# Performance work log

Hardware: AMD Instinct MI355X
Metric: run time of the kernel (lower is better)

Reference implementation:

```python
import jax, jax.numpy as jnp
import numpy as np

BOX = 100.0      # points live in [0, BOX)^3
STRIDE = 128     # > BOX/voxel_size, used for linearizing 3D voxel coords


def setup_inputs() -> dict:
    key = jax.random.key(0)
    k1, k2 = jax.random.split(key)
    N, C = 2_000_000, 32
    positions = jax.random.uniform(k1, (N, 3), dtype=jnp.float32) * BOX
    features = jax.random.normal(k2, (N, C), dtype=jnp.float32)
    voxel_size = jnp.ones((), dtype=jnp.float32)
    return {"positions": positions, "features": features, "voxel_size": voxel_size}


def reference(positions, features, voxel_size):
    """VoxelPooling(position_fn='center', feature_fn='max').

    Output is padded to N rows (M <= N real voxels); `valid` marks real voxels.
    Voxel grid is aligned to the origin; pooled position is the voxel center.
    """
    N = positions.shape[0]
    # integer voxel coordinates (positions are non-negative here)
    coords = jnp.floor(positions / voxel_size).astype(jnp.int32)           # [N,3]
    lin = coords[:, 0] + STRIDE * coords[:, 1] + STRIDE * STRIDE * coords[:, 2]  # [N]
    # compact unique voxels; jit-compatible with fixed size=N, pad with -1
    uniq, inv = jnp.unique(lin, size=N, fill_value=-1, return_inverse=True)
    # per-voxel max over features (empty segments get dtype-min, masked below)
    pooled_features = jax.ops.segment_max(features, inv, num_segments=N)   # [N,C]
    # decode voxel coords from linear key -> voxel centers
    cz = uniq // (STRIDE * STRIDE)
    rem = uniq % (STRIDE * STRIDE)
    cy = rem // STRIDE
    cx = rem % STRIDE
    centers = (jnp.stack([cx, cy, cz], axis=-1).astype(positions.dtype) + 0.5) * voxel_size
    valid = uniq >= 0                                                      # [N]
    pooled_positions = jnp.where(valid[:, None], centers, 0.0)
    pooled_features = jnp.where(valid[:, None], pooled_features, 0.0)
    return pooled_positions, pooled_features, valid
```

## Files before the change

kernel.cpp:

```cpp
#include <hip/hip_runtime.h>
#include <stdint.h>

#define STRIDE 128
#define NVOX (STRIDE * STRIDE * STRIDE)
#define BINVOX 512
#define NBIN (NVOX / BINVOX)
#define HB 256
#define HT 1024

typedef unsigned long long u64;

__device__ __forceinline__ uint32_t enc_f32(float f) {
  uint32_t u = __float_as_uint(f);
  return (u & 0x80000000u) ? ~u : (u | 0x80000000u);
}
__device__ __forceinline__ float dec_f32(uint32_t e) {
  uint32_t u = (e & 0x80000000u) ? (e & 0x7fffffffu) : ~e;
  return __uint_as_float(u);
}

__global__ __launch_bounds__(HT) void k_hist(const float* __restrict__ pos,
                                             const float* __restrict__ vs_p,
                                             int* __restrict__ lin_arr,
                                             uint32_t* __restrict__ hist, int n) {
  __shared__ uint32_t h[NBIN];
  int b = blockIdx.x, t = threadIdx.x;
  #pragma unroll
  for (int k = t; k < NBIN; k += HT) h[k] = 0u;
  __syncthreads();
  int chunk = (n + HB - 1) / HB;
  int i0 = b * chunk, i1 = min(n, i0 + chunk);
  float vs = vs_p[0];
  for (int i = i0 + t; i < i1; i += HT) {
    float x = pos[3 * (size_t)i + 0];
    float y = pos[3 * (size_t)i + 1];
    float z = pos[3 * (size_t)i + 2];
    int lin = (int)floorf(x / vs) + STRIDE * (int)floorf(y / vs) +
              STRIDE * STRIDE * (int)floorf(z / vs);
    lin_arr[i] = lin;
    atomicAdd(&h[lin >> 9], 1u);
  }
  __syncthreads();
  #pragma unroll
  for (int k = t; k < NBIN; k += HT) hist[(size_t)b * NBIN + k] = h[k];
}

__global__ void k_scanA(const uint32_t* __restrict__ hist, uint32_t* __restrict__ base2,
                        uint32_t* __restrict__ bin_tot) {
  int bin = blockIdx.x * blockDim.x + threadIdx.x;
  uint32_t run = 0;
  #pragma unroll 8
  for (int b = 0; b < HB; ++b) {
    uint32_t v = hist[(size_t)b * NBIN + bin];
    base2[(size_t)b * NBIN + bin] = run;
    run += v;
  }
  bin_tot[bin] = run;
}

__global__ __launch_bounds__(1024) void k_scan4k(const uint32_t* __restrict__ in,
                                                 uint32_t* __restrict__ out,
                                                 uint32_t* __restrict__ Mp) {
  __shared__ uint32_t s[1024];
  int t = threadIdx.x;
  uint32_t v[4], sum = 0;
  #pragma unroll
  for (int j = 0; j < 4; ++j) { v[j] = in[t * 4 + j]; sum += v[j]; }
  s[t] = sum;
  __syncthreads();
  for (int off = 1; off < 1024; off <<= 1) {
    uint32_t a = (t >= off) ? s[t - off] : 0u;
    __syncthreads();
    s[t] += a;
    __syncthreads();
  }
  uint32_t run = s[t] - sum;
  #pragma unroll
  for (int j = 0; j < 4; ++j) { out[t * 4 + j] = run; run += v[j]; }
  if (Mp != nullptr && t == 1023) Mp[0] = s[1023];
}

__global__ __launch_bounds__(HT) void k_part(const int* __restrict__ lin_arr,
                                             const uint32_t* __restrict__ bin_base,
                                             const uint32_t* __restrict__ base2,
                                             uint32_t* __restrict__ pairs, int n) {
  __shared__ uint32_t cur[NBIN];
  int b = blockIdx.x, t = threadIdx.x;
  #pragma unroll
  for (int k = t; k < NBIN; k += HT)
    cur[k] = bin_base[k] + base2[(size_t)b * NBIN + k];
  __syncthreads();
  int chunk = (n + HB - 1) / HB;
  int i0 = b * chunk, i1 = min(n, i0 + chunk);
  for (int i = i0 + t; i < i1; i += HT) {
    int lin = lin_arr[i];
    uint32_t slot = atomicAdd(&cur[lin >> 9], 1u);
    pairs[slot] = ((uint32_t)(lin & (BINVOX - 1)) << 21) | (uint32_t)i;
  }
}

__global__ void k_occ(const uint32_t* __restrict__ pairs,
                      const uint32_t* __restrict__ bin_base,
                      const uint32_t* __restrict__ bin_tot,
                      uint32_t* __restrict__ bins_bw, uint32_t* __restrict__ occ_cnt) {
  __shared__ uint32_t bw[16];
  int bin = blockIdx.x, t = threadIdx.x;
  if (t < 16) bw[t] = 0u;
  __syncthreads();
  uint32_t cnt = bin_tot[bin], start = bin_base[bin];
  for (uint32_t u = (uint32_t)t; u < cnt; u += blockDim.x) {
    uint32_t vb = pairs[start + u] >> 21;
    atomicOr(&bw[vb >> 5], 1u << (vb & 31));
  }
  __syncthreads();
  if (t < 16) bins_bw[(size_t)bin * 16 + t] = bw[t];
  if (t == 0) {
    uint32_t o = 0;
    #pragma unroll
    for (int w = 0; w < 16; ++w) o += __popc(bw[w]);
    occ_cnt[bin] = o;
  }
}

__global__ __launch_bounds__(1024) void k_pool(
    const float* __restrict__ feat, const float* __restrict__ vs_p,
    const uint32_t* __restrict__ pairs, const uint32_t* __restrict__ bin_base,
    const uint32_t* __restrict__ bin_tot, const uint32_t* __restrict__ occ_base,
    const uint32_t* __restrict__ bins_bw,
    float* __restrict__ out_pos, float* __restrict__ out_feat,
    float* __restrict__ out_valid) {
  __shared__ uint32_t smax[BINVOX * 32];
  __shared__ uint32_t sbw[16];
  int bin = blockIdx.x;
  int t = threadIdx.x;
  uint32_t cnt = bin_tot[bin];
  if (cnt == 0) return;
  uint32_t start = bin_base[bin];

  #pragma unroll
  for (int k = 0; k < 16; ++k) smax[t + k * 1024] = 0u;
  if (t < 16) sbw[t] = bins_bw[(size_t)bin * 16 + t];
  __syncthreads();

  int g = t >> 5;
  int ch = t & 31;
  uint32_t last = cnt - 1;
  for (uint32_t u = (uint32_t)g; u < cnt; u += 128) {
    uint32_t u1 = min(u + 32u, last), u2 = min(u + 64u, last), u3 = min(u + 96u, last);
    uint32_t p0 = pairs[start + u],  p1 = pairs[start + u1];
    uint32_t p2 = pairs[start + u2], p3 = pairs[start + u3];
    float v0 = feat[(size_t)(p0 & 0x1FFFFFu) * 32 + ch];
    float v1 = feat[(size_t)(p1 & 0x1FFFFFu) * 32 + ch];
    float v2 = feat[(size_t)(p2 & 0x1FFFFFu) * 32 + ch];
    float v3 = feat[(size_t)(p3 & 0x1FFFFFu) * 32 + ch];
    atomicMax(&smax[(p0 >> 21) * 32 + ch], enc_f32(v0));
    atomicMax(&smax[(p1 >> 21) * 32 + ch], enc_f32(v1));
    atomicMax(&smax[(p2 >> 21) * 32 + ch], enc_f32(v2));
    atomicMax(&smax[(p3 >> 21) * 32 + ch], enc_f32(v3));
  }
  __syncthreads();

  int vb = t >> 1, half = t & 1;
  uint32_t w = sbw[vb >> 5];
  uint32_t bit = (uint32_t)vb & 31u;
  if ((w >> bit) & 1u) {
    uint32_t lr = __popc(w & ((1u << bit) - 1u));
    for (int ww = 0; ww < (vb >> 5); ++ww) lr += __popc(sbw[ww]);
    uint32_t rank = occ_base[bin] + lr;
    float4* orow = (float4*)(out_feat + (size_t)rank * 32 + half * 16);
    #pragma unroll
    for (int j = 0; j < 4; ++j) {
      const uint32_t* sp = &smax[vb * 32 + half * 16 + j * 4];
      float4 o;
      o.x = dec_f32(sp[0]); o.y = dec_f32(sp[1]);
      o.z = dec_f32(sp[2]); o.w = dec_f32(sp[3]);
      orow[j] = o;
    }
    if (half == 0) {
      float vs = vs_p[0];
      int lin = bin * BINVOX + vb;
      int cx = lin & 127, cy = (lin >> 7) & 127, cz = lin >> 14;
      out_pos[(size_t)rank * 3 + 0] = ((float)cx + 0.5f) * vs;
      out_pos[(size_t)rank * 3 + 1] = ((float)cy + 0.5f) * vs;
      out_pos[(size_t)rank * 3 + 2] = ((float)cz + 0.5f) * vs;
      out_valid[rank] = 1.0f;
    }
  }
}

__global__ void k_tail(const uint32_t* __restrict__ Mp, float* __restrict__ out_pos,
                       float* __restrict__ out_feat, float* __restrict__ out_valid, int n) {
  size_t gid = (size_t)blockIdx.x * blockDim.x + threadIdx.x;
  int row = (int)(gid >> 3);
  int q = (int)(gid & 7);
  if (row >= n) return;
  uint32_t M = Mp[0];
  if ((uint32_t)row < M) return;
  ((float4*)out_feat)[(size_t)row * 8 + q] = make_float4(0.f, 0.f, 0.f, 0.f);
  if (q == 0) {
    out_pos[(size_t)row * 3 + 0] = 0.f;
    out_pos[(size_t)row * 3 + 1] = 0.f;
    out_pos[(size_t)row * 3 + 2] = 0.f;
    out_valid[row] = 0.f;
  }
}

extern "C" void kernel_launch(void* const* d_in, const int* in_sizes, int n_in,
                              void* d_out, int out_size, void* d_ws, size_t ws_size,
                              hipStream_t stream) {
  const float* pos  = (const float*)d_in[0];
  const float* feat = (const float*)d_in[1];
  const float* vs   = (const float*)d_in[2];
  int n = in_sizes[0] / 3;

  float*    out_pos   = (float*)d_out;
  uint32_t* out_feat  = (uint32_t*)(out_pos + (size_t)n * 3);
  float*    out_valid = (float*)((float*)out_feat + (size_t)n * 32);

  size_t scratch_u32 = 2 * (size_t)n + 2 * (size_t)HB * NBIN + 4 * (size_t)NBIN +
                       16 * (size_t)NBIN;
  uint32_t* scratch  = out_feat + (size_t)n * 32 - scratch_u32;
  int*      lin      = (int*)scratch;
  uint32_t* pairs    = scratch + n;
  uint32_t* hist     = pairs + n;
  uint32_t* base2    = hist + (size_t)HB * NBIN;
  uint32_t* bin_tot  = base2 + (size_t)HB * NBIN;
  uint32_t* bin_base = bin_tot + NBIN;
  uint32_t* occ_cnt  = bin_base + NBIN;
  uint32_t* occ_base = occ_cnt + NBIN;
  uint32_t* bins_bw  = occ_base + NBIN;

  uint32_t* Mp = (uint32_t*)d_ws;

  k_hist<<<HB, HT, 0, stream>>>(pos, vs, lin, hist, n);
  k_scanA<<<NBIN / 256, 256, 0, stream>>>(hist, base2, bin_tot);
  k_scan4k<<<1, 1024, 0, stream>>>(bin_tot, bin_base, nullptr);
  k_part<<<HB, HT, 0, stream>>>(lin, bin_base, base2, pairs, n);
  k_occ<<<NBIN, 256, 0, stream>>>(pairs, bin_base, bin_tot, bins_bw, occ_cnt);
  k_scan4k<<<1, 1024, 0, stream>>>(occ_cnt, occ_base, Mp);
  k_pool<<<NBIN, 1024, 0, stream>>>(feat, vs, pairs, bin_base, bin_tot, occ_base,
                                    bins_bw, out_pos, (float*)out_feat, out_valid);
  k_tail<<<(int)(((size_t)n * 8 + 255) / 256), 256, 0, stream>>>(
      Mp, out_pos, (float*)out_feat, out_valid, n);
}
```

Before: 230.7 us.

## Track voxel occupancy with a byte map and fuse both scans into one

Occupancy is now recorded in a per-voxel byte map written during the histogram pass. It is counted by popcount in the per-bin scan and rebuilt as 64-bit ballot masks in the pool kernel. This removes the separate k_occ pass over the pairs array and the second single-block scan, because bin counts and occupancy counts are packed into one 64-bit value and scanned together. The pool loop also unrolls to eight gathers per iteration for more memory-level parallelism. In exchange it adds a 2 MB memset and scattered byte writes in k_hist, plus higher register pressure in k_pool.

Result: faster. 225.0 us (-2.5%).

```diff
diff --git a/kernel.cpp b/kernel.cpp
--- a/kernel.cpp
+++ b/kernel.cpp
@@ -22,6 +22,7 @@
 __global__ __launch_bounds__(HT) void k_hist(const float* __restrict__ pos,
                                              const float* __restrict__ vs_p,
                                              int* __restrict__ lin_arr,
+                                             uint8_t* __restrict__ bytemap,
                                              uint32_t* __restrict__ hist, int n) {
   __shared__ uint32_t h[NBIN];
   int b = blockIdx.x, t = threadIdx.x;
@@ -38,6 +39,7 @@
     int lin = (int)floorf(x / vs) + STRIDE * (int)floorf(y / vs) +
               STRIDE * STRIDE * (int)floorf(z / vs);
     lin_arr[i] = lin;
+    bytemap[lin] = 1;
     atomicAdd(&h[lin >> 9], 1u);
   }
   __syncthreads();
@@ -45,39 +47,51 @@
   for (int k = t; k < NBIN; k += HT) hist[(size_t)b * NBIN + k] = h[k];
 }
 
-__global__ void k_scanA(const uint32_t* __restrict__ hist, uint32_t* __restrict__ base2,
-                        uint32_t* __restrict__ bin_tot) {
+__global__ void k_scanA(const uint32_t* __restrict__ hist,
+                        const uint32_t* __restrict__ bytemap_w,
+                        uint32_t* __restrict__ base2, u64* __restrict__ tot2) {
   int bin = blockIdx.x * blockDim.x + threadIdx.x;
   uint32_t run = 0;
   #pragma unroll 8
   for (int b = 0; b < HB; ++b) {
-    uint32_t v = hist[(size_t)b * NBIN + bin];
     base2[(size_t)b * NBIN + bin] = run;
-    run += v;
-  }
-  bin_tot[bin] = run;
-}
-
-__global__ __launch_bounds__(1024) void k_scan4k(const uint32_t* __restrict__ in,
-                                                 uint32_t* __restrict__ out,
+    run += hist[(size_t)b * NBIN + bin];
+  }
+  const uint4* bp = (const uint4*)(bytemap_w) + (size_t)bin * 32;
+  uint32_t occ = 0;
+  #pragma unroll
+  for (int k = 0; k < 32; ++k) {
+    uint4 v = bp[k];
+    occ += __popc(v.x) + __popc(v.y) + __popc(v.z) + __popc(v.w);
+  }
+  tot2[bin] = (u64)run | ((u64)occ << 32);
+}
+
+__global__ __launch_bounds__(1024) void k_scan64(const u64* __restrict__ in,
+                                                 uint32_t* __restrict__ bin_base,
+                                                 uint32_t* __restrict__ occ_base,
                                                  uint32_t* __restrict__ Mp) {
-  __shared__ uint32_t s[1024];
+  __shared__ u64 s[1024];
   int t = threadIdx.x;
-  uint32_t v[4], sum = 0;
+  u64 v[4], sum = 0;
   #pragma unroll
   for (int j = 0; j < 4; ++j) { v[j] = in[t * 4 + j]; sum += v[j]; }
   s[t] = sum;
   __syncthreads();
   for (int off = 1; off < 1024; off <<= 1) {
-    uint32_t a = (t >= off) ? s[t - off] : 0u;
+    u64 a = (t >= off) ? s[t - off] : 0ull;
     __syncthreads();
     s[t] += a;
     __syncthreads();
   }
-  uint32_t run = s[t] - sum;
-  #pragma unroll
-  for (int j = 0; j < 4; ++j) { out[t * 4 + j] = run; run += v[j]; }
-  if (Mp != nullptr && t == 1023) Mp[0] = s[1023];
+  u64 run = s[t] - sum;
+  #pragma unroll
+  for (int j = 0; j < 4; ++j) {
+    bin_base[t * 4 + j] = (uint32_t)run;
+    occ_base[t * 4 + j] = (uint32_t)(run >> 32);
+    run += v[j];
+  }
+  if (t == 1023) Mp[0] = (uint32_t)(s[1023] >> 32);
 }
 
 __global__ __launch_bounds__(HT) void k_part(const int* __restrict__ lin_arr,
@@ -99,73 +113,67 @@
   }
 }
 
-__global__ void k_occ(const uint32_t* __restrict__ pairs,
-                      const uint32_t* __restrict__ bin_base,
-                      const uint32_t* __restrict__ bin_tot,
-                      uint32_t* __restrict__ bins_bw, uint32_t* __restrict__ occ_cnt) {
-  __shared__ uint32_t bw[16];
-  int bin = blockIdx.x, t = threadIdx.x;
-  if (t < 16) bw[t] = 0u;
-  __syncthreads();
-  uint32_t cnt = bin_tot[bin], start = bin_base[bin];
-  for (uint32_t u = (uint32_t)t; u < cnt; u += blockDim.x) {
-    uint32_t vb = pairs[start + u] >> 21;
-    atomicOr(&bw[vb >> 5], 1u << (vb & 31));
-  }
-  __syncthreads();
-  if (t < 16) bins_bw[(size_t)bin * 16 + t] = bw[t];
-  if (t == 0) {
-    uint32_t o = 0;
-    #pragma unroll
-    for (int w = 0; w < 16; ++w) o += __popc(bw[w]);
-    occ_cnt[bin] = o;
-  }
-}
-
 __global__ __launch_bounds__(1024) void k_pool(
     const float* __restrict__ feat, const float* __restrict__ vs_p,
     const uint32_t* __restrict__ pairs, const uint32_t* __restrict__ bin_base,
-    const uint32_t* __restrict__ bin_tot, const uint32_t* __restrict__ occ_base,
-    const uint32_t* __restrict__ bins_bw,
+    const u64* __restrict__ tot2, const uint32_t* __restrict__ occ_base,
+    const uint8_t* __restrict__ bytemap,
     float* __restrict__ out_pos, float* __restrict__ out_feat,
     float* __restrict__ out_valid) {
   __shared__ uint32_t smax[BINVOX * 32];
-  __shared__ uint32_t sbw[16];
+  __shared__ u64 sbw[8];
   int bin = blockIdx.x;
   int t = threadIdx.x;
-  uint32_t cnt = bin_tot[bin];
+  uint32_t cnt = (uint32_t)tot2[bin];
   if (cnt == 0) return;
   uint32_t start = bin_base[bin];
 
   #pragma unroll
   for (int k = 0; k < 16; ++k) smax[t + k * 1024] = 0u;
-  if (t < 16) sbw[t] = bins_bw[(size_t)bin * 16 + t];
+  if (t < 512) {
+    uint32_t occb = bytemap[(size_t)bin * BINVOX + t];
+    u64 m = __ballot(occb != 0);
+    if ((t & 63) == 0) sbw[t >> 6] = m;
+  }
   __syncthreads();
 
   int g = t >> 5;
   int ch = t & 31;
   uint32_t last = cnt - 1;
-  for (uint32_t u = (uint32_t)g; u < cnt; u += 128) {
-    uint32_t u1 = min(u + 32u, last), u2 = min(u + 64u, last), u3 = min(u + 96u, last);
-    uint32_t p0 = pairs[start + u],  p1 = pairs[start + u1];
-    uint32_t p2 = pairs[start + u2], p3 = pairs[start + u3];
+  for (uint32_t u = (uint32_t)g; u < cnt; u += 256) {
+    uint32_t p0 = pairs[start + u];
+    uint32_t p1 = pairs[start + min(u + 32u, last)];
+    uint32_t p2 = pairs[start + min(u + 64u, last)];
+    uint32_t p3 = pairs[start + min(u + 96u, last)];
+    uint32_t p4 = pairs[start + min(u + 128u, last)];
+    uint32_t p5 = pairs[start + min(u + 160u, last)];
+    uint32_t p6 = pairs[start + min(u + 192u, last)];
+    uint32_t p7 = pairs[start + min(u + 224u, last)];
     float v0 = feat[(size_t)(p0 & 0x1FFFFFu) * 32 + ch];
     float v1 = feat[(size_t)(p1 & 0x1FFFFFu) * 32 + ch];
     float v2 = feat[(size_t)(p2 & 0x1FFFFFu) * 32 + ch];
     float v3 = feat[(size_t)(p3 & 0x1FFFFFu) * 32 + ch];
+    float v4 = feat[(size_t)(p4 & 0x1FFFFFu) * 32 + ch];
+    float v5 = feat[(size_t)(p5 & 0x1FFFFFu) * 32 + ch];
+    float v6 = feat[(size_t)(p6 & 0x1FFFFFu) * 32 + ch];
+    float v7 = feat[(size_t)(p7 & 0x1FFFFFu) * 32 + ch];
     atomicMax(&smax[(p0 >> 21) * 32 + ch], enc_f32(v0));
     atomicMax(&smax[(p1 >> 21) * 32 + ch], enc_f32(v1));
     atomicMax(&smax[(p2 >> 21) * 32 + ch], enc_f32(v2));
     atomicMax(&smax[(p3 >> 21) * 32 + ch], enc_f32(v3));
+    atomicMax(&smax[(p4 >> 21) * 32 + ch], enc_f32(v4));
+    atomicMax(&smax[(p5 >> 21) * 32 + ch], enc_f32(v5));
+    atomicMax(&smax[(p6 >> 21) * 32 + ch], enc_f32(v6));
+    atomicMax(&smax[(p7 >> 21) * 32 + ch], enc_f32(v7));
   }
   __syncthreads();
 
   int vb = t >> 1, half = t & 1;
-  uint32_t w = sbw[vb >> 5];
-  uint32_t bit = (uint32_t)vb & 31u;
-  if ((w >> bit) & 1u) {
-    uint32_t lr = __popc(w & ((1u << bit) - 1u));
-    for (int ww = 0; ww < (vb >> 5); ++ww) lr += __popc(sbw[ww]);
+  u64 w = sbw[vb >> 6];
+  int bit = vb & 63;
+  if ((w >> bit) & 1ull) {
+    uint32_t lr = (uint32_t)__popcll(w & ((1ull << bit) - 1ull));
+    for (int ww = 0; ww < (vb >> 6); ++ww) lr += (uint32_t)__popcll(sbw[ww]);
     uint32_t rank = occ_base[bin] + lr;
     float4* orow = (float4*)(out_feat + (size_t)rank * 32 + half * 16);
     #pragma unroll
@@ -217,29 +225,28 @@
   uint32_t* out_feat  = (uint32_t*)(out_pos + (size_t)n * 3);
   float*    out_valid = (float*)((float*)out_feat + (size_t)n * 32);
 
-  size_t scratch_u32 = 2 * (size_t)n + 2 * (size_t)HB * NBIN + 4 * (size_t)NBIN +
-                       16 * (size_t)NBIN;
+  size_t scratch_u32 = 2 * (size_t)n + 2 * (size_t)HB * NBIN + 2 * (size_t)NBIN +
+                       2 * (size_t)NBIN + NVOX / 4;
   uint32_t* scratch  = out_feat + (size_t)n * 32 - scratch_u32;
   int*      lin      = (int*)scratch;
   uint32_t* pairs    = scratch + n;
   uint32_t* hist     = pairs + n;
   uint32_t* base2    = hist + (size_t)HB * NBIN;
-  uint32_t* bin_tot  = base2 + (size_t)HB * NBIN;
-  uint32_t* bin_base = bin_tot + NBIN;
-  uint32_t* occ_cnt  = bin_base + NBIN;
-  uint32_t* occ_base = occ_cnt + NBIN;
-  uint32_t* bins_bw  = occ_base + NBIN;
+  u64*      tot2     = (u64*)(base2 + (size_t)HB * NBIN);
+  uint32_t* bin_base = (uint32_t*)(tot2 + NBIN);
+  uint32_t* occ_base = bin_base + NBIN;
+  uint8_t*  bytemap  = (uint8_t*)(occ_base + NBIN);
 
   uint32_t* Mp = (uint32_t*)d_ws;
 
-  k_hist<<<HB, HT, 0, stream>>>(pos, vs, lin, hist, n);
-  k_scanA<<<NBIN / 256, 256, 0, stream>>>(hist, base2, bin_tot);
-  k_scan4k<<<1, 1024, 0, stream>>>(bin_tot, bin_base, nullptr);
+  hipMemsetAsync(bytemap, 0, (size_t)NVOX, stream);
+
+  k_hist<<<HB, HT, 0, stream>>>(pos, vs, lin, bytemap, hist, n);
+  k_scanA<<<NBIN / 256, 256, 0, stream>>>(hist, (const uint32_t*)bytemap, base2, tot2);
+  k_scan64<<<1, 1024, 0, stream>>>(tot2, bin_base, occ_base, Mp);
   k_part<<<HB, HT, 0, stream>>>(lin, bin_base, base2, pairs, n);
-  k_occ<<<NBIN, 256, 0, stream>>>(pairs, bin_base, bin_tot, bins_bw, occ_cnt);
-  k_scan4k<<<1, 1024, 0, stream>>>(occ_cnt, occ_base, Mp);
-  k_pool<<<NBIN, 1024, 0, stream>>>(feat, vs, pairs, bin_base, bin_tot, occ_base,
-                                    bins_bw, out_pos, (float*)out_feat, out_valid);
+  k_pool<<<NBIN, 1024, 0, stream>>>(feat, vs, pairs, bin_base, tot2, occ_base,
+                                    bytemap, out_pos, (float*)out_feat, out_valid);
   k_tail<<<(int)(((size_t)n * 8 + 255) / 256), 256, 0, stream>>>(
       Mp, out_pos, (float*)out_feat, out_valid, n);
 }
```
